# Kernel optimization log

Measured on AMD Instinct MI355X. Metric: run time of the kernel, lower is better.

The kernel has to match this reference:

```python
import jax, jax.numpy as jnp
import numpy as np

SQRT_DIM = np.sqrt(64.0).astype(np.float32)


def setup_inputs() -> dict:
    key = jax.random.key(0)
    kq, kk, kv, km = jax.random.split(key, 4)
    B, H, S, D = 4, 16, 2048, 64
    q = jax.random.normal(kq, (B, H, S, D), dtype=jnp.float32)
    k = jax.random.normal(kk, (B, H, S, D), dtype=jnp.float32)
    v = jax.random.normal(kv, (B, H, S, D), dtype=jnp.float32)
    mask = jax.random.randint(km, (B, 1, S, S), 0, 2, dtype=jnp.int32)
    return {"q": q, "k": k, "v": v, "mask": mask}


def reference(q, k, v, mask):
    # scores: [B,H,S,S]
    scores = jnp.einsum('bhqd,bhkd->bhqk', q, k) / SQRT_DIM
    scores = jnp.where(mask == 0, jnp.float32(-1e9), scores)
    attn = jax.nn.softmax(scores, axis=-1)  # dropout p=0.0 -> identity
    output = jnp.einsum('bhqk,bhkd->bhqd', attn, v)
    return (output, attn)
```

## Files before the change

kernel.cpp:

```cpp
#include <hip/hip_runtime.h>

#define S_LEN 2048
#define DH 64
#define TQ 64
#define TK 64
#define NKT (S_LEN / TK)
#define LDSP 72

typedef __attribute__((ext_vector_type(8))) short short8;
typedef __attribute__((ext_vector_type(4))) short short4v;
typedef __attribute__((ext_vector_type(4))) float float4v;

static __device__ __forceinline__ short f2bf(float x) {
    unsigned u = __builtin_bit_cast(unsigned, x);
    u += 0x7fff + ((u >> 16) & 1);
    return (short)(u >> 16);
}

static __device__ __forceinline__ short8 cvt8(float4v a, float4v b) {
    short8 s;
    s[0] = f2bf(a[0]); s[1] = f2bf(a[1]); s[2] = f2bf(a[2]); s[3] = f2bf(a[3]);
    s[4] = f2bf(b[0]); s[5] = f2bf(b[1]); s[6] = f2bf(b[2]); s[7] = f2bf(b[3]);
    return s;
}

__global__ __launch_bounds__(256, 2) void attn_kernel(
    const float* __restrict__ q,
    const float* __restrict__ k,
    const float* __restrict__ v,
    const int*   __restrict__ mask,
    float* __restrict__ out,
    float* __restrict__ attn)
{
    __shared__ short Qs[TQ * LDSP];
    __shared__ short Ks[TK * LDSP];
    __shared__ short Vt[DH * LDSP];
    __shared__ short Ps[4 * 16 * LDSP];

    const int tid  = threadIdx.x;
    const int wave = tid >> 6;
    const int lane = tid & 63;
    const int l16  = lane & 15;
    const int quad = lane >> 4;

    const int bid = blockIdx.x;
    const int qt  = bid & 31;
    const int bh  = bid >> 5;
    const int b   = bh >> 4;
    const int q0  = qt * TQ;

    const float* qg = q + ((size_t)bh * S_LEN + q0) * DH;
    const float* kg = k + (size_t)bh * S_LEN * DH;
    const float* vg = v + (size_t)bh * S_LEN * DH;
    const int*   mg = mask + ((size_t)b * S_LEN + q0) * S_LEN;
    float* attng = attn + ((size_t)bh * S_LEN + q0) * (size_t)S_LEN;

    const int qrow_base = wave * 16;

    #pragma unroll
    for (int it = 0; it < 2; ++it) {
        int c = tid + it * 256;
        int row = c >> 3, col8 = (c & 7) << 3;
        const float4v* gp = (const float4v*)(qg + (size_t)row * DH + col8);
        *(short8*)&Qs[row * LDSP + col8] = cvt8(gp[0], gp[1]);
    }

    auto stageK = [&](int kt) {
        #pragma unroll
        for (int it = 0; it < 2; ++it) {
            int c = tid + it * 256;
            int row = c >> 3, col8 = (c & 7) << 3;
            const float4v* gp = (const float4v*)(kg + (size_t)(kt * TK + row) * DH + col8);
            *(short8*)&Ks[row * LDSP + col8] = cvt8(gp[0], gp[1]);
        }
    };

    float rs[4] = {0.f, 0.f, 0.f, 0.f};

    for (int kt = 0; kt < NKT; ++kt) {
        __syncthreads();
        stageK(kt);
        __syncthreads();

        short8 afr0 = *(const short8*)&Qs[(qrow_base + l16) * LDSP + quad * 8];
        short8 afr1 = *(const short8*)&Qs[(qrow_base + l16) * LDSP + 32 + quad * 8];

        #pragma unroll
        for (int sub = 0; sub < 4; ++sub) {
            float4v acc = {0.f, 0.f, 0.f, 0.f};
            short8 b0 = *(const short8*)&Ks[(sub * 16 + l16) * LDSP + quad * 8];
            short8 b1 = *(const short8*)&Ks[(sub * 16 + l16) * LDSP + 32 + quad * 8];
            acc = __builtin_amdgcn_mfma_f32_16x16x32_bf16(afr0, b0, acc, 0, 0, 0);
            acc = __builtin_amdgcn_mfma_f32_16x16x32_bf16(afr1, b1, acc, 0, 0, 0);
            int kkg = kt * TK + sub * 16 + l16;
            #pragma unroll
            for (int r = 0; r < 4; ++r) {
                int qrow = qrow_base + quad * 4 + r;
                int m = mg[(size_t)qrow * S_LEN + kkg];
                float p = m ? __expf(acc[r] * 0.125f) : 0.f;
                rs[r] += p;
            }
        }
    }

    #pragma unroll
    for (int r = 0; r < 4; ++r) {
        float s = rs[r];
        s += __shfl_xor(s, 1);
        s += __shfl_xor(s, 2);
        s += __shfl_xor(s, 4);
        s += __shfl_xor(s, 8);
        rs[r] = 1.0f / s;
    }

    float4v oacc[4];
    #pragma unroll
    for (int i = 0; i < 4; ++i) oacc[i] = (float4v){0.f, 0.f, 0.f, 0.f};

    short* Pw = &Ps[wave * 16 * LDSP];

    for (int kt = 0; kt < NKT; ++kt) {
        __syncthreads();
        stageK(kt);
        {
            int kb = tid >> 4, db = tid & 15;
            const float* vbase = vg + (size_t)(kt * TK + kb * 4) * DH + db * 4;
            float4v r0 = *(const float4v*)(vbase + 0 * DH);
            float4v r1 = *(const float4v*)(vbase + 1 * DH);
            float4v r2 = *(const float4v*)(vbase + 2 * DH);
            float4v r3 = *(const float4v*)(vbase + 3 * DH);
            #pragma unroll
            for (int t = 0; t < 4; ++t) {
                int i = (t + tid) & 3;
                short4v sv = { f2bf(r0[i]), f2bf(r1[i]), f2bf(r2[i]), f2bf(r3[i]) };
                *(short4v*)&Vt[(db * 4 + i) * LDSP + kb * 4] = sv;
            }
        }
        __syncthreads();

        short8 afr0 = *(const short8*)&Qs[(qrow_base + l16) * LDSP + quad * 8];
        short8 afr1 = *(const short8*)&Qs[(qrow_base + l16) * LDSP + 32 + quad * 8];

        #pragma unroll
        for (int sub = 0; sub < 4; ++sub) {
            float4v acc = {0.f, 0.f, 0.f, 0.f};
            short8 b0 = *(const short8*)&Ks[(sub * 16 + l16) * LDSP + quad * 8];
            short8 b1 = *(const short8*)&Ks[(sub * 16 + l16) * LDSP + 32 + quad * 8];
            acc = __builtin_amdgcn_mfma_f32_16x16x32_bf16(afr0, b0, acc, 0, 0, 0);
            acc = __builtin_amdgcn_mfma_f32_16x16x32_bf16(afr1, b1, acc, 0, 0, 0);
            int kkl = sub * 16 + l16;
            int kkg = kt * TK + kkl;
            #pragma unroll
            for (int r = 0; r < 4; ++r) {
                int qrow = qrow_base + quad * 4 + r;
                int m = mg[(size_t)qrow * S_LEN + kkg];
                float p = m ? __expf(acc[r] * 0.125f) * rs[r] : 0.f;
                attng[(size_t)qrow * S_LEN + kkg] = p;
                Pw[(quad * 4 + r) * LDSP + kkl] = f2bf(p);
            }
        }
        __syncthreads();

        #pragma unroll
        for (int ks = 0; ks < 2; ++ks) {
            short8 pa = *(const short8*)&Pw[l16 * LDSP + ks * 32 + quad * 8];
            #pragma unroll
            for (int dsub = 0; dsub < 4; ++dsub) {
                short8 bv = *(const short8*)&Vt[(dsub * 16 + l16) * LDSP + ks * 32 + quad * 8];
                oacc[dsub] = __builtin_amdgcn_mfma_f32_16x16x32_bf16(pa, bv, oacc[dsub], 0, 0, 0);
            }
        }
    }

    float* og = out + ((size_t)bh * S_LEN + q0) * DH;
    #pragma unroll
    for (int dsub = 0; dsub < 4; ++dsub) {
        #pragma unroll
        for (int r = 0; r < 4; ++r) {
            og[(size_t)(qrow_base + quad * 4 + r) * DH + dsub * 16 + l16] = oacc[dsub][r];
        }
    }
}

extern "C" void kernel_launch(void* const* d_in, const int* in_sizes, int n_in,
                              void* d_out, int out_size, void* d_ws, size_t ws_size,
                              hipStream_t stream) {
    (void)in_sizes; (void)n_in; (void)out_size; (void)d_ws; (void)ws_size;
    const float* q    = (const float*)d_in[0];
    const float* k    = (const float*)d_in[1];
    const float* v    = (const float*)d_in[2];
    const int*   mask = (const int*)d_in[3];
    float* out  = (float*)d_out;
    float* attn = out + (size_t)4 * 16 * 2048 * 64;
    attn_kernel<<<dim3(2048), dim3(256), 0, stream>>>(q, k, v, mask, out, attn);
}
```

Before: 1.556 ms.

## Double-buffer K/V tiles, register-prefetch mask, keep P in registers with vectorized attn stores

Double-buffers the K and V LDS tiles and prefetches the next tile's K, V and mask into registers while the current tile's MFMAs run, with one barrier per iteration. It swaps the MFMA operands and permutes K rows so each lane holds contiguous key columns of one query row. That lets mask loads be int4 vectors and attn writes be float4 nontemporal stores, and P feeds the PV MFMA directly from registers without an LDS round trip. Q is now loaded once into registers instead of LDS. The cost is higher register pressure and custom barrier code that depends on a permuted-row layout being correct.

```diff
diff --git a/kernel.cpp b/kernel.cpp
--- a/kernel.cpp
+++ b/kernel.cpp
@@ -2,7 +2,6 @@
 
 #define S_LEN 2048
 #define DH 64
-#define TQ 64
 #define TK 64
 #define NKT (S_LEN / TK)
 #define LDSP 72
@@ -10,6 +9,7 @@
 typedef __attribute__((ext_vector_type(8))) short short8;
 typedef __attribute__((ext_vector_type(4))) short short4v;
 typedef __attribute__((ext_vector_type(4))) float float4v;
+typedef __attribute__((ext_vector_type(4))) int   int4v;
 
 static __device__ __forceinline__ short f2bf(float x) {
     unsigned u = __builtin_bit_cast(unsigned, x);
@@ -22,6 +22,13 @@
     s[0] = f2bf(a[0]); s[1] = f2bf(a[1]); s[2] = f2bf(a[2]); s[3] = f2bf(a[3]);
     s[4] = f2bf(b[0]); s[5] = f2bf(b[1]); s[6] = f2bf(b[2]); s[7] = f2bf(b[3]);
     return s;
+}
+
+static __device__ __forceinline__ void tile_barrier() {
+    asm volatile("s_waitcnt lgkmcnt(0)" ::: "memory");
+    __builtin_amdgcn_s_barrier();
+    __builtin_amdgcn_sched_barrier(0);
+    asm volatile("" ::: "memory");
 }
 
 __global__ __launch_bounds__(256, 2) void attn_kernel(
@@ -32,10 +39,8 @@
     float* __restrict__ out,
     float* __restrict__ attn)
 {
-    __shared__ short Qs[TQ * LDSP];
-    __shared__ short Ks[TK * LDSP];
-    __shared__ short Vt[DH * LDSP];
-    __shared__ short Ps[4 * 16 * LDSP];
+    __shared__ short Ks[2][TK * LDSP];
+    __shared__ short Vt[2][DH * LDSP];
 
     const int tid  = threadIdx.x;
     const int wave = tid >> 6;
@@ -47,7 +52,7 @@
     const int qt  = bid & 31;
     const int bh  = bid >> 5;
     const int b   = bh >> 4;
-    const int q0  = qt * TQ;
+    const int q0  = qt * TK;
 
     const float* qg = q + ((size_t)bh * S_LEN + q0) * DH;
     const float* kg = k + (size_t)bh * S_LEN * DH;
@@ -55,121 +60,163 @@
     const int*   mg = mask + ((size_t)b * S_LEN + q0) * S_LEN;
     float* attng = attn + ((size_t)bh * S_LEN + q0) * (size_t)S_LEN;
 
-    const int qrow_base = wave * 16;
-
-    #pragma unroll
-    for (int it = 0; it < 2; ++it) {
-        int c = tid + it * 256;
-        int row = c >> 3, col8 = (c & 7) << 3;
-        const float4v* gp = (const float4v*)(qg + (size_t)row * DH + col8);
-        *(short8*)&Qs[row * LDSP + col8] = cvt8(gp[0], gp[1]);
+    const int qrow = wave * 16 + l16;
+
+    const int krow0 = tid >> 3;
+    const int kcol8 = (tid & 7) << 3;
+    auto permrow = [](int kk) {
+        return ((kk & 4) << 2) | (kk & 32) | ((kk & 24) >> 1) | (kk & 3);
+    };
+    const int kpr0 = permrow(krow0);
+    const int kpr1 = permrow(krow0 + 32);
+    const int vkb = tid >> 4, vdb = tid & 15;
+
+    float4v ks0a, ks0b, ks1a, ks1b;
+    float4v vr0, vr1, vr2, vr3;
+
+    auto loadK = [&](int kt) {
+        const float* p0 = kg + (size_t)(kt * TK + krow0) * DH + kcol8;
+        ks0a = *(const float4v*)(p0);
+        ks0b = *(const float4v*)(p0 + 4);
+        const float* p1 = p0 + 32 * DH;
+        ks1a = *(const float4v*)(p1);
+        ks1b = *(const float4v*)(p1 + 4);
+    };
+    auto writeK = [&](int buf) {
+        *(short8*)&Ks[buf][kpr0 * LDSP + kcol8] = cvt8(ks0a, ks0b);
+        *(short8*)&Ks[buf][kpr1 * LDSP + kcol8] = cvt8(ks1a, ks1b);
+    };
+    auto loadV = [&](int kt) {
+        const float* vb = vg + (size_t)(kt * TK + vkb * 4) * DH + vdb * 4;
+        vr0 = *(const float4v*)(vb);
+        vr1 = *(const float4v*)(vb + DH);
+        vr2 = *(const float4v*)(vb + 2 * DH);
+        vr3 = *(const float4v*)(vb + 3 * DH);
+    };
+    auto writeV = [&](int buf) {
+        #pragma unroll
+        for (int t = 0; t < 4; ++t) {
+            int i = (t + tid) & 3;
+            short4v sv = { f2bf(vr0[i]), f2bf(vr1[i]), f2bf(vr2[i]), f2bf(vr3[i]) };
+            *(short4v*)&Vt[buf][(vdb * 4 + i) * LDSP + vkb * 4] = sv;
+        }
+    };
+
+    const float* qp = qg + (size_t)qrow * DH + quad * 8;
+    float4v qa0 = *(const float4v*)(qp);
+    float4v qa1 = *(const float4v*)(qp + 4);
+    float4v qb0 = *(const float4v*)(qp + 32);
+    float4v qb1 = *(const float4v*)(qp + 36);
+    loadK(0);
+    short8 afr0 = cvt8(qa0, qa1);
+    short8 afr1 = cvt8(qb0, qb1);
+    writeK(0);
+
+    const int* mrow = mg + (size_t)qrow * S_LEN;
+    int4v mk[4], mkn[4];
+    #pragma unroll
+    for (int s = 0; s < 4; ++s)
+        mk[s] = *(const int4v*)(mrow + ((s >> 1) << 5) + (quad << 3) + ((s & 1) << 2));
+
+    tile_barrier();
+
+    float rs = 0.f;
+    for (int kt = 0; kt < NKT; ++kt) {
+        const int cur = kt & 1;
+        if (kt + 1 < NKT) {
+            loadK(kt + 1);
+            #pragma unroll
+            for (int s = 0; s < 4; ++s)
+                mkn[s] = *(const int4v*)(mrow + (kt + 1) * TK +
+                          ((s >> 1) << 5) + (quad << 3) + ((s & 1) << 2));
+        } else {
+            loadK(0);
+            loadV(0);
+        }
+        #pragma unroll
+        for (int s = 0; s < 4; ++s) {
+            float4v acc = {0.f, 0.f, 0.f, 0.f};
+            const short* kr = &Ks[cur][(s * 16 + l16) * LDSP + quad * 8];
+            short8 b0 = *(const short8*)(kr);
+            short8 b1 = *(const short8*)(kr + 32);
+            acc = __builtin_amdgcn_mfma_f32_16x16x32_bf16(b0, afr0, acc, 0, 0, 0);
+            acc = __builtin_amdgcn_mfma_f32_16x16x32_bf16(b1, afr1, acc, 0, 0, 0);
+            #pragma unroll
+            for (int r = 0; r < 4; ++r)
+                rs += mk[s][r] ? __expf(acc[r] * 0.125f) : 0.f;
+        }
+        if (kt + 1 < NKT) {
+            writeK(cur ^ 1);
+            #pragma unroll
+            for (int s = 0; s < 4; ++s) mk[s] = mkn[s];
+        } else {
+            writeK(cur ^ 1);
+            writeV(cur ^ 1);
+        }
+        tile_barrier();
     }
 
-    auto stageK = [&](int kt) {
-        #pragma unroll
-        for (int it = 0; it < 2; ++it) {
-            int c = tid + it * 256;
-            int row = c >> 3, col8 = (c & 7) << 3;
-            const float4v* gp = (const float4v*)(kg + (size_t)(kt * TK + row) * DH + col8);
-            *(short8*)&Ks[row * LDSP + col8] = cvt8(gp[0], gp[1]);
-        }
-    };
-
-    float rs[4] = {0.f, 0.f, 0.f, 0.f};
+    #pragma unroll
+    for (int s = 0; s < 4; ++s)
+        mk[s] = *(const int4v*)(mrow + ((s >> 1) << 5) + (quad << 3) + ((s & 1) << 2));
+    rs += __shfl_xor(rs, 16);
+    rs += __shfl_xor(rs, 32);
+    rs = 1.0f / rs;
+
+    float4v oacc[4];
+    #pragma unroll
+    for (int i = 0; i < 4; ++i) oacc[i] = (float4v){0.f, 0.f, 0.f, 0.f};
+    float* arow = attng + (size_t)qrow * S_LEN;
 
     for (int kt = 0; kt < NKT; ++kt) {
-        __syncthreads();
-        stageK(kt);
-        __syncthreads();
-
-        short8 afr0 = *(const short8*)&Qs[(qrow_base + l16) * LDSP + quad * 8];
-        short8 afr1 = *(const short8*)&Qs[(qrow_base + l16) * LDSP + 32 + quad * 8];
-
-        #pragma unroll
-        for (int sub = 0; sub < 4; ++sub) {
+        const int cur = kt & 1;
+        if (kt + 1 < NKT) {
+            loadK(kt + 1);
+            loadV(kt + 1);
+            #pragma unroll
+            for (int s = 0; s < 4; ++s)
+                mkn[s] = *(const int4v*)(mrow + (kt + 1) * TK +
+                          ((s >> 1) << 5) + (quad << 3) + ((s & 1) << 2));
+        }
+        float p[4][4];
+        #pragma unroll
+        for (int s = 0; s < 4; ++s) {
             float4v acc = {0.f, 0.f, 0.f, 0.f};
-            short8 b0 = *(const short8*)&Ks[(sub * 16 + l16) * LDSP + quad * 8];
-            short8 b1 = *(const short8*)&Ks[(sub * 16 + l16) * LDSP + 32 + quad * 8];
-            acc = __builtin_amdgcn_mfma_f32_16x16x32_bf16(afr0, b0, acc, 0, 0, 0);
-            acc = __builtin_amdgcn_mfma_f32_16x16x32_bf16(afr1, b1, acc, 0, 0, 0);
-            int kkg = kt * TK + sub * 16 + l16;
+            const short* kr = &Ks[cur][(s * 16 + l16) * LDSP + quad * 8];
+            short8 b0 = *(const short8*)(kr);
+            short8 b1 = *(const short8*)(kr + 32);
+            acc = __builtin_amdgcn_mfma_f32_16x16x32_bf16(b0, afr0, acc, 0, 0, 0);
+            acc = __builtin_amdgcn_mfma_f32_16x16x32_bf16(b1, afr1, acc, 0, 0, 0);
+            float4v pv;
             #pragma unroll
             for (int r = 0; r < 4; ++r) {
-                int qrow = qrow_base + quad * 4 + r;
-                int m = mg[(size_t)qrow * S_LEN + kkg];
-                float p = m ? __expf(acc[r] * 0.125f) : 0.f;
-                rs[r] += p;
+                float pe = mk[s][r] ? __expf(acc[r] * 0.125f) * rs : 0.f;
+                p[s][r] = pe;
+                pv[r] = pe;
             }
-        }
-    }
-
-    #pragma unroll
-    for (int r = 0; r < 4; ++r) {
-        float s = rs[r];
-        s += __shfl_xor(s, 1);
-        s += __shfl_xor(s, 2);
-        s += __shfl_xor(s, 4);
-        s += __shfl_xor(s, 8);
-        rs[r] = 1.0f / s;
-    }
-
-    float4v oacc[4];
-    #pragma unroll
-    for (int i = 0; i < 4; ++i) oacc[i] = (float4v){0.f, 0.f, 0.f, 0.f};
-
-    short* Pw = &Ps[wave * 16 * LDSP];
-
-    for (int kt = 0; kt < NKT; ++kt) {
-        __syncthreads();
-        stageK(kt);
-        {
-            int kb = tid >> 4, db = tid & 15;
-            const float* vbase = vg + (size_t)(kt * TK + kb * 4) * DH + db * 4;
-            float4v r0 = *(const float4v*)(vbase + 0 * DH);
-            float4v r1 = *(const float4v*)(vbase + 1 * DH);
-            float4v r2 = *(const float4v*)(vbase + 2 * DH);
-            float4v r3 = *(const float4v*)(vbase + 3 * DH);
-            #pragma unroll
-            for (int t = 0; t < 4; ++t) {
-                int i = (t + tid) & 3;
-                short4v sv = { f2bf(r0[i]), f2bf(r1[i]), f2bf(r2[i]), f2bf(r3[i]) };
-                *(short4v*)&Vt[(db * 4 + i) * LDSP + kb * 4] = sv;
-            }
-        }
-        __syncthreads();
-
-        short8 afr0 = *(const short8*)&Qs[(qrow_base + l16) * LDSP + quad * 8];
-        short8 afr1 = *(const short8*)&Qs[(qrow_base + l16) * LDSP + 32 + quad * 8];
-
-        #pragma unroll
-        for (int sub = 0; sub < 4; ++sub) {
-            float4v acc = {0.f, 0.f, 0.f, 0.f};
-            short8 b0 = *(const short8*)&Ks[(sub * 16 + l16) * LDSP + quad * 8];
-            short8 b1 = *(const short8*)&Ks[(sub * 16 + l16) * LDSP + 32 + quad * 8];
-            acc = __builtin_amdgcn_mfma_f32_16x16x32_bf16(afr0, b0, acc, 0, 0, 0);
-            acc = __builtin_amdgcn_mfma_f32_16x16x32_bf16(afr1, b1, acc, 0, 0, 0);
-            int kkl = sub * 16 + l16;
-            int kkg = kt * TK + kkl;
-            #pragma unroll
-            for (int r = 0; r < 4; ++r) {
-                int qrow = qrow_base + quad * 4 + r;
-                int m = mg[(size_t)qrow * S_LEN + kkg];
-                float p = m ? __expf(acc[r] * 0.125f) * rs[r] : 0.f;
-                attng[(size_t)qrow * S_LEN + kkg] = p;
-                Pw[(quad * 4 + r) * LDSP + kkl] = f2bf(p);
-            }
-        }
-        __syncthreads();
-
+            __builtin_nontemporal_store(pv,
+                (float4v*)(arow + kt * TK + ((s >> 1) << 5) + (quad << 3) + ((s & 1) << 2)));
+        }
         #pragma unroll
         for (int ks = 0; ks < 2; ++ks) {
-            short8 pa = *(const short8*)&Pw[l16 * LDSP + ks * 32 + quad * 8];
+            short8 pa;
+            pa[0] = f2bf(p[2 * ks][0]);     pa[1] = f2bf(p[2 * ks][1]);
+            pa[2] = f2bf(p[2 * ks][2]);     pa[3] = f2bf(p[2 * ks][3]);
+            pa[4] = f2bf(p[2 * ks + 1][0]); pa[5] = f2bf(p[2 * ks + 1][1]);
+            pa[6] = f2bf(p[2 * ks + 1][2]); pa[7] = f2bf(p[2 * ks + 1][3]);
             #pragma unroll
             for (int dsub = 0; dsub < 4; ++dsub) {
-                short8 bv = *(const short8*)&Vt[(dsub * 16 + l16) * LDSP + ks * 32 + quad * 8];
+                short8 bv = *(const short8*)&Vt[cur][(dsub * 16 + l16) * LDSP + ks * 32 + quad * 8];
                 oacc[dsub] = __builtin_amdgcn_mfma_f32_16x16x32_bf16(pa, bv, oacc[dsub], 0, 0, 0);
             }
         }
+        if (kt + 1 < NKT) {
+            writeK(cur ^ 1);
+            writeV(cur ^ 1);
+            #pragma unroll
+            for (int s = 0; s < 4; ++s) mk[s] = mkn[s];
+        }
+        tile_barrier();
     }
 
     float* og = out + ((size_t)bh * S_LEN + q0) * DH;
@@ -177,7 +224,7 @@
     for (int dsub = 0; dsub < 4; ++dsub) {
         #pragma unroll
         for (int r = 0; r < 4; ++r) {
-            og[(size_t)(qrow_base + quad * 4 + r) * DH + dsub * 16 + l16] = oacc[dsub][r];
+            og[(size_t)(wave * 16 + quad * 4 + r) * DH + dsub * 16 + l16] = oacc[dsub][r];
         }
     }
 }
```

New measurement: 1.528 ms. About the same (-1.8%).
